# Optimization experiments

Hardware: AMD Instinct MI355X
Metric: run time of the kernel (lower is better)

Reference implementation:

```python
import jax, jax.numpy as jnp
import numpy as np

N = 100000      # nodes
E = 1600000     # directed edges (before self-loops)
IN = 128        # in_channels
H = 4           # heads
C = 32          # out_channels per head
SLOPE = 0.2     # PyG GATConv default negative_slope


def setup_inputs() -> dict:
    key = jax.random.key(0)
    k_x, k_e, k_w, k_as, k_ad = jax.random.split(key, 5)
    x = jax.random.normal(k_x, (N, IN), dtype=jnp.float32)
    edge_index = jax.random.randint(k_e, (2, E), 0, N, dtype=jnp.int32)
    # learned params of GATConv(IN, C, heads=H, concat=False)
    W = jax.random.normal(k_w, (IN, H * C), dtype=jnp.float32) / np.sqrt(IN)
    att_src = jax.random.normal(k_as, (H, C), dtype=jnp.float32) * 0.1
    att_dst = jax.random.normal(k_ad, (H, C), dtype=jnp.float32) * 0.1
    bias = jnp.zeros((C,), dtype=jnp.float32)
    return {"x": x, "edge_index": edge_index, "W": W,
            "att_src": att_src, "att_dst": att_dst, "bias": bias}


def reference(x, edge_index, W, att_src, att_dst, bias):
    # PyG GATConv default add_self_loops=True
    loops = jnp.arange(N, dtype=edge_index.dtype)
    src = jnp.concatenate([edge_index[0], loops])  # message sources j
    dst = jnp.concatenate([edge_index[1], loops])  # message targets i

    # linear projection per head: [N, H, C]
    xp = (x @ W).reshape(N, H, C)

    # per-node attention logits: [N, H]
    a_src = jnp.einsum('nhc,hc->nh', xp, att_src)
    a_dst = jnp.einsum('nhc,hc->nh', xp, att_dst)

    # per-edge logits + leaky relu: [E', H]
    e = jax.nn.leaky_relu(a_src[src] + a_dst[dst], SLOPE)

    # segment softmax over incoming edges of each destination node
    e_max = jax.ops.segment_max(e, dst, num_segments=N)          # [N, H]
    e_exp = jnp.exp(e - e_max[dst])                              # [E', H]
    denom = jax.ops.segment_sum(e_exp, dst, num_segments=N)      # [N, H]
    alpha = e_exp / denom[dst]                                   # [E', H]
    # (attention dropout p=0.6 is inactive in eval mode)

    # weighted scatter-add aggregation: [N, H, C]
    msg = alpha[:, :, None] * xp[src]
    out = jax.ops.segment_sum(msg, dst, num_segments=N)

    # concat=False -> mean over heads, then bias; GATLayer applies relu
    out = out.mean(axis=1) + bias
    return jax.nn.relu(out)
```

## Files before the change

kernel.cpp:

```cpp
#include <hip/hip_runtime.h>
#include <cstdint>
#include <cstddef>

#define NNODE 100000
#define NEDGE 1600000
#define INC   128
#define HC    128
#define NH    4
#define CPH   32
#define NPART 8
#define NP8   (NNODE * NPART)
#define SLOPE 0.2f
#define KP    136

#define LRELU(v) fmaxf((v), SLOPE*(v))

typedef _Float16 half4 __attribute__((ext_vector_type(4)));
typedef _Float16 half2v __attribute__((ext_vector_type(2)));
typedef _Float16 f16x8 __attribute__((ext_vector_type(8)));
typedef float    f32x4 __attribute__((ext_vector_type(4)));

static inline size_t align256(size_t x){ return (x + 255) & ~(size_t)255; }

__global__ void wprep_kernel(const float* __restrict__ W, _Float16* __restrict__ wt16)
{
    const int idx = blockIdx.x * 256 + threadIdx.x;
    const int k = idx >> 7, c = idx & 127;
    wt16[c * 128 + k] = (_Float16)W[k * 128 + c];
}

__global__ __launch_bounds__(256) void proj_kernel(
    const float* __restrict__ x, const _Float16* __restrict__ wt16,
    _Float16* __restrict__ xp16)
{
    __shared__ _Float16 wt_s[128 * KP];
    __shared__ _Float16 x_s[64 * KP];

    const int tid  = threadIdx.x;
    const int lane = tid & 63;
    const int w    = tid >> 6;
    const int row0 = blockIdx.x * 64;

    #pragma unroll
    for (int i = 0; i < 16; ++i) {
        const int idx = i * 256 + tid;
        const int r = idx >> 5, c4 = idx & 31;
        *(half4*)(wt_s + r * KP + c4 * 4) = *(const half4*)(wt16 + r * 128 + c4 * 4);
    }
    #pragma unroll
    for (int i = 0; i < 8; ++i) {
        const int idx = i * 256 + tid;
        const int r = idx >> 5, c4 = idx & 31;
        const int row = row0 + r;
        half4 hv;
        if (row < NNODE) {
            const float4 v = *(const float4*)(x + (size_t)row * INC + c4 * 4);
            hv = half4{(_Float16)v.x, (_Float16)v.y, (_Float16)v.z, (_Float16)v.w};
        } else {
            hv = half4{(_Float16)0.f, (_Float16)0.f, (_Float16)0.f, (_Float16)0.f};
        }
        *(half4*)(x_s + r * KP + c4 * 4) = hv;
    }
    __syncthreads();

    const int l15 = lane & 15;
    const int q   = lane >> 4;

    f32x4 acc[8];
    #pragma unroll
    for (int n = 0; n < 8; ++n) acc[n] = f32x4{0.f, 0.f, 0.f, 0.f};

    #pragma unroll
    for (int kc = 0; kc < 4; ++kc) {
        const f16x8 a = *(const f16x8*)(x_s + (16 * w + l15) * KP + kc * 32 + q * 8);
        #pragma unroll
        for (int n = 0; n < 8; ++n) {
            const f16x8 b = *(const f16x8*)(wt_s + (16 * n + l15) * KP + kc * 32 + q * 8);
            acc[n] = __builtin_amdgcn_mfma_f32_16x16x32_f16(a, b, acc[n], 0, 0, 0);
        }
    }

    __syncthreads();
    #pragma unroll
    for (int n = 0; n < 8; ++n)
        #pragma unroll
        for (int r = 0; r < 4; ++r)
            x_s[(16 * w + q * 4 + r) * KP + 16 * n + l15] = (_Float16)acc[n][r];
    __syncthreads();

    #pragma unroll
    for (int i = 0; i < 8; ++i) {
        const int idx = i * 256 + tid;
        const int r = idx >> 5, c4 = idx & 31;
        const int row = row0 + r;
        if (row < NNODE)
            *(half4*)(xp16 + (size_t)row * HC + c4 * 4) = *(const half4*)(x_s + r * KP + c4 * 4);
    }
}

__global__ __launch_bounds__(256) void logits_kernel(
    const _Float16* __restrict__ xp16, const float* __restrict__ att_src,
    const float* __restrict__ att_dst, float* __restrict__ a_src,
    float* __restrict__ a_dst)
{
    const int lane = threadIdx.x & 63;
    const int wid  = threadIdx.x >> 6;
    const int node = blockIdx.x * 4 + wid;
    if (node >= NNODE) return;

    const half2v xh = *(const half2v*)(xp16 + (size_t)node * HC + 2 * lane);
    const float x0 = (float)xh[0], x1 = (float)xh[1];
    const float2 as = ((const float2*)att_src)[lane];
    const float2 ad = ((const float2*)att_dst)[lane];
    float s = x0 * as.x + x1 * as.y;
    float d = x0 * ad.x + x1 * ad.y;
    #pragma unroll
    for (int off = 8; off; off >>= 1) {
        s += __shfl_xor(s, off);
        d += __shfl_xor(d, off);
    }
    if ((lane & 15) == 0) {
        const int h = lane >> 4;
        a_src[(size_t)node * NH + h] = s;
        a_dst[(size_t)node * NH + h] = d;
    }
}

__global__ void count_seq_kernel(const int* __restrict__ ei,
                                 int* __restrict__ deg,
                                 int* __restrict__ seq)
{
    const int t4 = (blockIdx.x * 256 + threadIdx.x) * 4;
    const int p = blockIdx.x & (NPART - 1);
    if (t4 < NEDGE) {
        const int4 d4 = *(const int4*)(ei + NEDGE + t4);
        int4 s4;
        s4.x = atomicAdd(&deg[p * NNODE + d4.x], 1);
        s4.y = atomicAdd(&deg[p * NNODE + d4.y], 1);
        s4.z = atomicAdd(&deg[p * NNODE + d4.z], 1);
        s4.w = atomicAdd(&deg[p * NNODE + d4.w], 1);
        *(int4*)(seq + t4) = s4;
    }
}

__global__ __launch_bounds__(256) void scan_sums_kernel(
    const int* __restrict__ deg, int* __restrict__ bsums)
{
    __shared__ int lds[4];
    const int tid = threadIdx.x, lane = tid & 63, wid = tid >> 6;
    const int base = blockIdx.x * 4096 + tid * 16;
    int s = 0;
    #pragma unroll
    for (int i = 0; i < 16; ++i) {
        const int idx = base + i;
        if (idx < NP8) s += deg[idx];
    }
    #pragma unroll
    for (int off = 32; off; off >>= 1) s += __shfl_xor(s, off);
    if (lane == 0) lds[wid] = s;
    __syncthreads();
    if (tid == 0) bsums[blockIdx.x] = lds[0] + lds[1] + lds[2] + lds[3];
}

__global__ __launch_bounds__(256) void scan_partials_kernel(
    int* __restrict__ bsums, int nb)
{
    __shared__ int lds[4];
    const int tid = threadIdx.x, lane = tid & 63, wid = tid >> 6;
    const int v = (tid < nb) ? bsums[tid] : 0;
    int incl = v;
    #pragma unroll
    for (int off = 1; off < 64; off <<= 1) {
        const int u = __shfl_up(incl, off);
        if (lane >= off) incl += u;
    }
    if (lane == 63) lds[wid] = incl;
    __syncthreads();
    int wb = 0;
    for (int w = 0; w < wid; ++w) wb += lds[w];
    if (tid < nb) bsums[tid] = wb + incl - v;
}

__global__ __launch_bounds__(256) void scan_final_kernel(
    const int* __restrict__ deg, const int* __restrict__ bsums,
    int* __restrict__ offs)
{
    __shared__ int lds[4];
    const int tid = threadIdx.x, lane = tid & 63, wid = tid >> 6;
    const int base = blockIdx.x * 4096 + tid * 16;
    int v[16]; int s = 0;
    #pragma unroll
    for (int i = 0; i < 16; ++i) {
        const int idx = base + i;
        v[i] = (idx < NP8) ? deg[idx] : 0;
        s += v[i];
    }
    int incl = s;
    #pragma unroll
    for (int off = 1; off < 64; off <<= 1) {
        const int u = __shfl_up(incl, off);
        if (lane >= off) incl += u;
    }
    if (lane == 63) lds[wid] = incl;
    __syncthreads();
    int wb = 0;
    for (int w = 0; w < wid; ++w) wb += lds[w];
    int excl = bsums[blockIdx.x] + wb + incl - s;
    #pragma unroll
    for (int i = 0; i < 16; ++i) {
        const int idx = base + i;
        if (idx < NP8) offs[idx] = excl;
        excl += v[i];
    }
    if (blockIdx.x == 0 && tid == 0) offs[NP8] = NEDGE;
}

__global__ void scatter_kernel(const int* __restrict__ ei,
                               const int* __restrict__ offs,
                               const int* __restrict__ seq,
                               int* __restrict__ csr)
{
    const int t4 = (blockIdx.x * 256 + threadIdx.x) * 4;
    const int p = blockIdx.x & (NPART - 1);
    if (t4 < NEDGE) {
        const int4 d4 = *(const int4*)(ei + NEDGE + t4);
        const int4 s4 = *(const int4*)(ei + t4);
        const int4 q4 = *(const int4*)(seq + t4);
        csr[offs[p * NNODE + d4.x] + q4.x] = s4.x;
        csr[offs[p * NNODE + d4.y] + q4.y] = s4.y;
        csr[offs[p * NNODE + d4.z] + q4.z] = s4.z;
        csr[offs[p * NNODE + d4.w] + q4.w] = s4.w;
    }
}

__global__ __launch_bounds__(256) void aggregate_kernel(
    const _Float16* __restrict__ xp16, const float* __restrict__ a_src,
    const float* __restrict__ a_dst, const int* __restrict__ offs,
    const int* __restrict__ csr, const float* __restrict__ bias,
    float* __restrict__ out)
{
    __shared__ float p_lds[4][2][32][4];
    __shared__ int   j_lds[4][2][32];

    const int lane = threadIdx.x & 63;
    const int wid  = threadIdx.x >> 6;
    const int half = lane >> 5;
    const int sl   = lane & 31;
    const int node = blockIdx.x * 8 + wid * 2 + half;
    const int h    = sl >> 3;

    int s_val = 0, len = 0;
    if (sl < 8) {
        const int o0 = offs[sl * NNODE + node];
        const int o1 = offs[sl * NNODE + node + 1];
        s_val = o0; len = o1 - o0;
    }
    int incl = len;
    #pragma unroll
    for (int o = 1; o < 8; o <<= 1) {
        const int u = __shfl_up(incl, o, 32);
        if (sl >= o) incl += u;
    }
    const int excl = incl - len;
    int s_arr[8], b_arr[8];
    #pragma unroll
    for (int q = 0; q < 8; ++q) {
        s_arr[q] = __shfl(s_val, q, 32);
        b_arr[q] = __shfl(excl,  q, 32);
    }
    const int D = __shfl(incl, 7, 32);

    const float4 ad = ((const float4*)a_dst)[node];
    const float4 as = ((const float4*)a_src)[node];

    const float lself = (h == 0) ? LRELU(as.x + ad.x)
                      : (h == 1) ? LRELU(as.y + ad.y)
                      : (h == 2) ? LRELU(as.z + ad.z)
                                 : LRELU(as.w + ad.w);
    const float pself = __expf(lself);
    float den = pself;
    float4 acc;
    {
        const half4 hv = *(const half4*)(xp16 + (size_t)node * HC + 4 * sl);
        acc.x = pself * (float)hv.x; acc.y = pself * (float)hv.y;
        acc.z = pself * (float)hv.z; acc.w = pself * (float)hv.w;
    }

    float* pme = &p_lds[wid][half][sl][0];
    int*   jme = &j_lds[wid][half][sl];
    const float* pw = &p_lds[wid][half][0][h];
    const int*   jw = &j_lds[wid][half][0];

    for (int base = 0; base < D; base += 32) {
        const int cnt = min(32, D - base);
        if (sl < cnt) {
            const int v = base + sl;
            int sp = s_arr[0], ex = b_arr[0];
            #pragma unroll
            for (int q = 1; q < 8; ++q) {
                const bool c = (v >= b_arr[q]);
                sp = c ? s_arr[q] : sp;
                ex = c ? b_arr[q] : ex;
            }
            const int j = csr[sp + v - ex];
            const float4 aj = ((const float4*)a_src)[j];
            const float p0 = __expf(LRELU(aj.x + ad.x));
            const float p1 = __expf(LRELU(aj.y + ad.y));
            const float p2 = __expf(LRELU(aj.z + ad.z));
            const float p3 = __expf(LRELU(aj.w + ad.w));
            *(float4*)pme = make_float4(p0, p1, p2, p3);
            *jme = j;
        }

        asm volatile("s_waitcnt lgkmcnt(0)" ::: "memory");

        int t = 0;
        for (; t + 3 < cnt; t += 4) {
            const int j0 = jw[t], j1 = jw[t+1], j2 = jw[t+2], j3 = jw[t+3];
            const float q0 = pw[4*t], q1 = pw[4*t+4], q2 = pw[4*t+8], q3 = pw[4*t+12];
            const half4 v0 = *(const half4*)(xp16 + (size_t)j0 * HC + 4 * sl);
            const half4 v1 = *(const half4*)(xp16 + (size_t)j1 * HC + 4 * sl);
            const half4 v2 = *(const half4*)(xp16 + (size_t)j2 * HC + 4 * sl);
            const half4 v3 = *(const half4*)(xp16 + (size_t)j3 * HC + 4 * sl);
            den += q0 + q1 + q2 + q3;
            acc.x = fmaf(q0, (float)v0.x, acc.x); acc.y = fmaf(q0, (float)v0.y, acc.y);
            acc.z = fmaf(q0, (float)v0.z, acc.z); acc.w = fmaf(q0, (float)v0.w, acc.w);
            acc.x = fmaf(q1, (float)v1.x, acc.x); acc.y = fmaf(q1, (float)v1.y, acc.y);
            acc.z = fmaf(q1, (float)v1.z, acc.z); acc.w = fmaf(q1, (float)v1.w, acc.w);
            acc.x = fmaf(q2, (float)v2.x, acc.x); acc.y = fmaf(q2, (float)v2.y, acc.y);
            acc.z = fmaf(q2, (float)v2.z, acc.z); acc.w = fmaf(q2, (float)v2.w, acc.w);
            acc.x = fmaf(q3, (float)v3.x, acc.x); acc.y = fmaf(q3, (float)v3.y, acc.y);
            acc.z = fmaf(q3, (float)v3.z, acc.z); acc.w = fmaf(q3, (float)v3.w, acc.w);
        }
        for (; t < cnt; ++t) {
            const int   jt = jw[t];
            const float pt = pw[4*t];
            const half4 hv = *(const half4*)(xp16 + (size_t)jt * HC + 4 * sl);
            den += pt;
            acc.x = fmaf(pt, (float)hv.x, acc.x); acc.y = fmaf(pt, (float)hv.y, acc.y);
            acc.z = fmaf(pt, (float)hv.z, acc.z); acc.w = fmaf(pt, (float)hv.w, acc.w);
        }
    }

    const float inv = 1.0f / den;
    float4 r;
    r.x = acc.x * inv; r.y = acc.y * inv; r.z = acc.z * inv; r.w = acc.w * inv;
    r.x += __shfl_xor(r.x, 8); r.x += __shfl_xor(r.x, 16);
    r.y += __shfl_xor(r.y, 8); r.y += __shfl_xor(r.y, 16);
    r.z += __shfl_xor(r.z, 8); r.z += __shfl_xor(r.z, 16);
    r.w += __shfl_xor(r.w, 8); r.w += __shfl_xor(r.w, 16);
    if (sl < 8) {
        const float4 b = ((const float4*)bias)[sl];
        float4 o;
        o.x = fmaxf(0.25f * r.x + b.x, 0.f);
        o.y = fmaxf(0.25f * r.y + b.y, 0.f);
        o.z = fmaxf(0.25f * r.z + b.z, 0.f);
        o.w = fmaxf(0.25f * r.w + b.w, 0.f);
        *(float4*)(out + (size_t)node * CPH + 4 * sl) = o;
    }
}

extern "C" void kernel_launch(void* const* d_in, const int* in_sizes, int n_in,
                              void* d_out, int out_size, void* d_ws, size_t ws_size,
                              hipStream_t stream)
{
    const float* x       = (const float*)d_in[0];
    const int*   ei      = (const int*)d_in[1];
    const float* W       = (const float*)d_in[2];
    const float* att_src = (const float*)d_in[3];
    const float* att_dst = (const float*)d_in[4];
    const float* bias    = (const float*)d_in[5];
    float*       out     = (float*)d_out;

    char* ws = (char*)d_ws;
    size_t off = 0;
    auto alloc = [&](size_t bytes) -> void* {
        void* p = ws + off;
        off = align256(off + bytes);
        return p;
    };
    _Float16* xp16 = (_Float16*)alloc((size_t)NNODE * HC * sizeof(_Float16));
    _Float16* wt16 = (_Float16*)alloc((size_t)HC * INC * sizeof(_Float16));
    float* a_src  = (float*)alloc((size_t)NNODE * NH * sizeof(float));
    float* a_dst  = (float*)alloc((size_t)NNODE * NH * sizeof(float));
    int*   deg    = (int*)alloc((size_t)NP8 * sizeof(int));
    int*   seq    = (int*)alloc((size_t)NEDGE * sizeof(int));
    int*   offs   = (int*)alloc((size_t)(NP8 + 1) * sizeof(int));
    int*   csr    = (int*)alloc((size_t)NEDGE * sizeof(int));
    int*   bsums  = (int*)alloc(1024);

    hipMemsetAsync(deg, 0, (size_t)NP8 * sizeof(int), stream);

    wprep_kernel<<<64, 256, 0, stream>>>(W, wt16);
    proj_kernel<<<(NNODE + 63) / 64, 256, 0, stream>>>(x, wt16, xp16);
    logits_kernel<<<(NNODE + 3) / 4, 256, 0, stream>>>(xp16, att_src, att_dst, a_src, a_dst);

    constexpr int EB = (NEDGE / 4 + 255) / 256;
    count_seq_kernel<<<EB, 256, 0, stream>>>(ei, deg, seq);

    constexpr int NB = (NP8 + 4095) / 4096;
    scan_sums_kernel<<<NB, 256, 0, stream>>>(deg, bsums);
    scan_partials_kernel<<<1, 256, 0, stream>>>(bsums, NB);
    scan_final_kernel<<<NB, 256, 0, stream>>>(deg, bsums, offs);

    scatter_kernel<<<EB, 256, 0, stream>>>(ei, offs, seq, csr);
    aggregate_kernel<<<NNODE / 8, 256, 0, stream>>>(xp16, a_src, a_dst, offs, csr, bias, out);
}
```

Measured before the change: 295.4 us.

## Fuse attention logits into projection kernel and make it persistent

The separate logits kernel is removed. Attention source and destination logits are now computed inside the projection kernel from the fp32 MFMA accumulators, using shuffle reductions, which avoids re-reading xp16 and one kernel launch. The projection kernel also becomes a grid-stride persistent kernel with 512 blocks, so the W tile is loaded into LDS once per block instead of once per 64-row chunk. The cost is extra shuffle work per chunk and fewer blocks, which may reduce latency hiding. Logits now come from fp32 accumulators rather than rounded fp16 values, a slight numerical difference.

Result: slower. 303.6 us (+2.8%).

```diff
diff --git a/kernel.cpp b/kernel.cpp
--- a/kernel.cpp
+++ b/kernel.cpp
@@ -12,11 +12,11 @@
 #define NP8   (NNODE * NPART)
 #define SLOPE 0.2f
 #define KP    136
+#define NCHUNK ((NNODE + 63) / 64)
 
 #define LRELU(v) fmaxf((v), SLOPE*(v))
 
 typedef _Float16 half4 __attribute__((ext_vector_type(4)));
-typedef _Float16 half2v __attribute__((ext_vector_type(2)));
 typedef _Float16 f16x8 __attribute__((ext_vector_type(8)));
 typedef float    f32x4 __attribute__((ext_vector_type(4)));
 
@@ -31,7 +31,9 @@
 
 __global__ __launch_bounds__(256) void proj_kernel(
     const float* __restrict__ x, const _Float16* __restrict__ wt16,
-    _Float16* __restrict__ xp16)
+    const float* __restrict__ att_src, const float* __restrict__ att_dst,
+    _Float16* __restrict__ xp16, float* __restrict__ a_src,
+    float* __restrict__ a_dst)
 {
     __shared__ _Float16 wt_s[128 * KP];
     __shared__ _Float16 x_s[64 * KP];
@@ -39,7 +41,8 @@
     const int tid  = threadIdx.x;
     const int lane = tid & 63;
     const int w    = tid >> 6;
-    const int row0 = blockIdx.x * 64;
+    const int l15  = lane & 15;
+    const int q    = lane >> 4;
 
     #pragma unroll
     for (int i = 0; i < 16; ++i) {
@@ -47,82 +50,84 @@
         const int r = idx >> 5, c4 = idx & 31;
         *(half4*)(wt_s + r * KP + c4 * 4) = *(const half4*)(wt16 + r * 128 + c4 * 4);
     }
-    #pragma unroll
-    for (int i = 0; i < 8; ++i) {
-        const int idx = i * 256 + tid;
-        const int r = idx >> 5, c4 = idx & 31;
-        const int row = row0 + r;
-        half4 hv;
-        if (row < NNODE) {
-            const float4 v = *(const float4*)(x + (size_t)row * INC + c4 * 4);
-            hv = half4{(_Float16)v.x, (_Float16)v.y, (_Float16)v.z, (_Float16)v.w};
-        } else {
-            hv = half4{(_Float16)0.f, (_Float16)0.f, (_Float16)0.f, (_Float16)0.f};
-        }
-        *(half4*)(x_s + r * KP + c4 * 4) = hv;
-    }
-    __syncthreads();
-
-    const int l15 = lane & 15;
-    const int q   = lane >> 4;
-
-    f32x4 acc[8];
-    #pragma unroll
-    for (int n = 0; n < 8; ++n) acc[n] = f32x4{0.f, 0.f, 0.f, 0.f};
-
-    #pragma unroll
-    for (int kc = 0; kc < 4; ++kc) {
-        const f16x8 a = *(const f16x8*)(x_s + (16 * w + l15) * KP + kc * 32 + q * 8);
-        #pragma unroll
-        for (int n = 0; n < 8; ++n) {
-            const f16x8 b = *(const f16x8*)(wt_s + (16 * n + l15) * KP + kc * 32 + q * 8);
-            acc[n] = __builtin_amdgcn_mfma_f32_16x16x32_f16(a, b, acc[n], 0, 0, 0);
-        }
-    }
-
-    __syncthreads();
-    #pragma unroll
-    for (int n = 0; n < 8; ++n)
-        #pragma unroll
-        for (int r = 0; r < 4; ++r)
-            x_s[(16 * w + q * 4 + r) * KP + 16 * n + l15] = (_Float16)acc[n][r];
-    __syncthreads();
-
-    #pragma unroll
-    for (int i = 0; i < 8; ++i) {
-        const int idx = i * 256 + tid;
-        const int r = idx >> 5, c4 = idx & 31;
-        const int row = row0 + r;
-        if (row < NNODE)
-            *(half4*)(xp16 + (size_t)row * HC + c4 * 4) = *(const half4*)(x_s + r * KP + c4 * 4);
-    }
-}
-
-__global__ __launch_bounds__(256) void logits_kernel(
-    const _Float16* __restrict__ xp16, const float* __restrict__ att_src,
-    const float* __restrict__ att_dst, float* __restrict__ a_src,
-    float* __restrict__ a_dst)
-{
-    const int lane = threadIdx.x & 63;
-    const int wid  = threadIdx.x >> 6;
-    const int node = blockIdx.x * 4 + wid;
-    if (node >= NNODE) return;
-
-    const half2v xh = *(const half2v*)(xp16 + (size_t)node * HC + 2 * lane);
-    const float x0 = (float)xh[0], x1 = (float)xh[1];
-    const float2 as = ((const float2*)att_src)[lane];
-    const float2 ad = ((const float2*)att_dst)[lane];
-    float s = x0 * as.x + x1 * as.y;
-    float d = x0 * ad.x + x1 * ad.y;
-    #pragma unroll
-    for (int off = 8; off; off >>= 1) {
-        s += __shfl_xor(s, off);
-        d += __shfl_xor(d, off);
-    }
-    if ((lane & 15) == 0) {
-        const int h = lane >> 4;
-        a_src[(size_t)node * NH + h] = s;
-        a_dst[(size_t)node * NH + h] = d;
+
+    float ats[8], atd[8];
+    #pragma unroll
+    for (int n = 0; n < 8; ++n) {
+        ats[n] = att_src[16 * n + l15];
+        atd[n] = att_dst[16 * n + l15];
+    }
+
+    for (int chunk = blockIdx.x; chunk < NCHUNK; chunk += gridDim.x) {
+        const int row0 = chunk * 64;
+        __syncthreads();
+
+        #pragma unroll
+        for (int i = 0; i < 8; ++i) {
+            const int idx = i * 256 + tid;
+            const int r = idx >> 5, c4 = idx & 31;
+            const int row = row0 + r;
+            half4 hv;
+            if (row < NNODE) {
+                const float4 v = *(const float4*)(x + (size_t)row * INC + c4 * 4);
+                hv = half4{(_Float16)v.x, (_Float16)v.y, (_Float16)v.z, (_Float16)v.w};
+            } else {
+                hv = half4{(_Float16)0.f, (_Float16)0.f, (_Float16)0.f, (_Float16)0.f};
+            }
+            *(half4*)(x_s + r * KP + c4 * 4) = hv;
+        }
+        __syncthreads();
+
+        f32x4 acc[8];
+        #pragma unroll
+        for (int n = 0; n < 8; ++n) acc[n] = f32x4{0.f, 0.f, 0.f, 0.f};
+
+        #pragma unroll
+        for (int kc = 0; kc < 4; ++kc) {
+            const f16x8 a = *(const f16x8*)(x_s + (16 * w + l15) * KP + kc * 32 + q * 8);
+            #pragma unroll
+            for (int n = 0; n < 8; ++n) {
+                const f16x8 b = *(const f16x8*)(wt_s + (16 * n + l15) * KP + kc * 32 + q * 8);
+                acc[n] = __builtin_amdgcn_mfma_f32_16x16x32_f16(a, b, acc[n], 0, 0, 0);
+            }
+        }
+
+        #pragma unroll
+        for (int h = 0; h < 4; ++h) {
+            #pragma unroll
+            for (int r = 0; r < 4; ++r) {
+                float s = acc[2*h][r] * ats[2*h] + acc[2*h+1][r] * ats[2*h+1];
+                float d = acc[2*h][r] * atd[2*h] + acc[2*h+1][r] * atd[2*h+1];
+                s += __shfl_xor(s, 1); s += __shfl_xor(s, 2);
+                s += __shfl_xor(s, 4); s += __shfl_xor(s, 8);
+                d += __shfl_xor(d, 1); d += __shfl_xor(d, 2);
+                d += __shfl_xor(d, 4); d += __shfl_xor(d, 8);
+                if (l15 == 0) {
+                    const int row = row0 + 16 * w + q * 4 + r;
+                    if (row < NNODE) {
+                        a_src[(size_t)row * NH + h] = s;
+                        a_dst[(size_t)row * NH + h] = d;
+                    }
+                }
+            }
+        }
+
+        __syncthreads();
+        #pragma unroll
+        for (int n = 0; n < 8; ++n)
+            #pragma unroll
+            for (int r = 0; r < 4; ++r)
+                x_s[(16 * w + q * 4 + r) * KP + 16 * n + l15] = (_Float16)acc[n][r];
+        __syncthreads();
+
+        #pragma unroll
+        for (int i = 0; i < 8; ++i) {
+            const int idx = i * 256 + tid;
+            const int r = idx >> 5, c4 = idx & 31;
+            const int row = row0 + r;
+            if (row < NNODE)
+                *(half4*)(xp16 + (size_t)row * HC + c4 * 4) = *(const half4*)(x_s + r * KP + c4 * 4);
+        }
     }
 }
 
@@ -392,8 +397,7 @@
     hipMemsetAsync(deg, 0, (size_t)NP8 * sizeof(int), stream);
 
     wprep_kernel<<<64, 256, 0, stream>>>(W, wt16);
-    proj_kernel<<<(NNODE + 63) / 64, 256, 0, stream>>>(x, wt16, xp16);
-    logits_kernel<<<(NNODE + 3) / 4, 256, 0, stream>>>(xp16, att_src, att_dst, a_src, a_dst);
+    proj_kernel<<<512, 256, 0, stream>>>(x, wt16, att_src, att_dst, xp16, a_src, a_dst);
 
     constexpr int EB = (NEDGE / 4 + 255) / 256;
     count_seq_kernel<<<EB, 256, 0, stream>>>(ei, deg, seq);
```
